# Performance work log

Hardware: AMD Instinct MI355X
Metric: run time of the kernel (lower is better)

Reference implementation:

```python
import jax, jax.numpy as jnp
import numpy as np

IN_DIM = 128
OUT_DIM = 128
NUM_RELS = 8
N_NODES = 50000
N_EDGES = 500000


def setup_inputs() -> dict:
    key = jax.random.key(0)
    k_x, k_ei_s, k_ei_d, k_et, k_w, k_sw = jax.random.split(key, 6)
    x = jax.random.normal(k_x, (N_NODES, IN_DIM), dtype=jnp.float32)
    src = jax.random.randint(k_ei_s, (N_EDGES,), 0, N_NODES)
    dst = jax.random.randint(k_ei_d, (N_EDGES,), 0, N_NODES)
    edge_index = jnp.stack([src, dst], axis=0).astype(jnp.int64)
    edge_type = jax.random.randint(k_et, (N_EDGES,), 0, NUM_RELS).astype(jnp.int64)
    # xavier_uniform: bound = sqrt(6/(fan_in+fan_out))
    bw = float(np.sqrt(6.0 / (IN_DIM + OUT_DIM)))
    weight = jax.random.uniform(k_w, (NUM_RELS, IN_DIM, OUT_DIM), dtype=jnp.float32, minval=-bw, maxval=bw)
    self_loop_weight = jax.random.uniform(k_sw, (IN_DIM, OUT_DIM), dtype=jnp.float32, minval=-bw, maxval=bw)
    bias = jnp.zeros((OUT_DIM,), dtype=jnp.float32)
    return {
        "x": x,
        "weight": weight,
        "self_loop_weight": self_loop_weight,
        "bias": bias,
        "edge_index": edge_index,
        "edge_type": edge_type,
        "num_entities": N_NODES,
    }


def reference(x, weight, self_loop_weight, bias, edge_index, edge_type, num_entities):
    # Relation-grouped formulation of the per-edge loop:
    # transform every node under every relation once: hr[r, n, o]
    hr = jnp.einsum("nd,rdo->rno", x, weight)
    src, dst = edge_index[0], edge_index[1]
    # per-edge message = x[src] @ weight[edge_type]  == hr[edge_type, src]
    msg = hr[edge_type, src]  # [E, out]
    agg = jax.ops.segment_sum(msg, dst, num_segments=num_entities)  # scatter-add into out[dst]
    out = agg + x @ self_loop_weight + bias
    return jax.nn.relu(out)
```

## Files before the change

kernel.cpp:

```cpp
#include <hip/hip_runtime.h>

#define IN_DIM 128
#define OUT_DIM 128
#define NUM_RELS 8
#define SCAN_ELEMS 2048

typedef unsigned short u16;
typedef u16 u16x8 __attribute__((ext_vector_type(8)));
typedef u16 u16x4 __attribute__((ext_vector_type(4)));
typedef __bf16 bf16x8 __attribute__((ext_vector_type(8)));
typedef float f32x4 __attribute__((ext_vector_type(4)));

__device__ __forceinline__ u16 f2bf(float f) {
    unsigned u = __float_as_uint(f);
    u += 0x7FFF + ((u >> 16) & 1);
    return (u16)(u >> 16);
}
__device__ __forceinline__ float bf2f(u16 h) {
    return __uint_as_float((unsigned)h << 16);
}

__global__ __launch_bounds__(256) void k_prep(
    const float* __restrict__ x, const float* __restrict__ weight,
    const float* __restrict__ slw,
    const int* __restrict__ dst, const int* __restrict__ et,
    u16* __restrict__ xb, u16* __restrict__ WbT, int* __restrict__ cursor,
    int N, int E, int BA, int BB)
{
    const int b = blockIdx.x;
    const int tid = threadIdx.x;
    if (b < BA) {
        long i = ((long)b * 256 + tid) * 4;
        if (i < (long)N * 128) {
            float4 v = *(const float4*)(x + i);
            u16x4 o;
            o[0] = f2bf(v.x); o[1] = f2bf(v.y); o[2] = f2bf(v.z); o[3] = f2bf(v.w);
            *(u16x4*)(xb + i) = o;
        }
    } else if (b < BA + BB) {
        int i = ((b - BA) * 256 + tid) * 4;
        if (i < 128 * 1152) {
            const int col = i / 1152;
            const int kk  = i - col * 1152;
            u16x4 o;
            #pragma unroll
            for (int j = 0; j < 4; ++j) {
                const int kj = kk + j;
                const float f = (kj < 1024)
                    ? weight[((kj >> 7) << 14) + ((kj & 127) << 7) + col]
                    : slw[((kj - 1024) << 7) + col];
                o[j] = f2bf(f);
            }
            *(u16x4*)(WbT + i) = o;
        }
    } else {
        int e = (b - BA - BB) * 256 + tid;
        if (e < E) atomicAdd(&cursor[(dst[e] << 3) + et[e]], 1);
    }
}

__global__ __launch_bounds__(256) void k_scan1(
    const int* __restrict__ deg, int* __restrict__ local,
    int* __restrict__ bsum, int n)
{
    __shared__ int s[256];
    const int t = threadIdx.x;
    const int base = blockIdx.x * SCAN_ELEMS + t * 8;
    int v[8];
    int sum = 0;
    #pragma unroll
    for (int j = 0; j < 8; ++j) {
        int i = base + j;
        v[j] = (i < n) ? deg[i] : 0;
        sum += v[j];
    }
    s[t] = sum;
    __syncthreads();
    #pragma unroll
    for (int off = 1; off < 256; off <<= 1) {
        int y = (t >= off) ? s[t - off] : 0;
        __syncthreads();
        s[t] += y;
        __syncthreads();
    }
    int run = s[t] - sum;
    #pragma unroll
    for (int j = 0; j < 8; ++j) {
        int i = base + j;
        if (i < n) local[i] = run;
        run += v[j];
    }
    if (t == 255) bsum[blockIdx.x] = s[255];
}

__global__ __launch_bounds__(256) void k_scan23(
    int* __restrict__ row_ptr, const int* __restrict__ bsum,
    int* __restrict__ cursor, int B, int n)
{
    __shared__ int s[256];
    const int t = threadIdx.x;
    int v = (t < B) ? bsum[t] : 0;
    s[t] = v;
    __syncthreads();
    #pragma unroll
    for (int off = 1; off < 256; off <<= 1) {
        int y = (t >= off) ? s[t - off] : 0;
        __syncthreads();
        s[t] += y;
        __syncthreads();
    }
    const int myoff = (blockIdx.x == 0) ? 0 : s[blockIdx.x - 1];
    const int total = s[255];
    const int base = blockIdx.x * SCAN_ELEMS + t * 8;
    #pragma unroll
    for (int j = 0; j < 8; ++j) {
        int i = base + j;
        if (i < n) {
            int val = row_ptr[i] + myoff;
            row_ptr[i] = val;
            cursor[i] = val;
        }
    }
    if (blockIdx.x == 0 && t == 0) row_ptr[n] = total;
}

__global__ __launch_bounds__(256) void k_fill(
    const int* __restrict__ src, const int* __restrict__ dst,
    const int* __restrict__ et, int* __restrict__ cursor,
    int* __restrict__ packed, int E)
{
    int e = blockIdx.x * blockDim.x + threadIdx.x;
    if (e >= E) return;
    int pos = atomicAdd(&cursor[(dst[e] << 3) + et[e]], 1);
    packed[pos] = (et[e] << 17) | src[e];
}

#define NPB 32
#define LDK 392

__global__ __launch_bounds__(512, 8) void fused_rgcn(
    const u16* __restrict__ xb,
    const u16* __restrict__ WbT,
    const float* __restrict__ bias,
    const int* __restrict__ row_ptr,
    const int* __restrict__ packed,
    float* __restrict__ out, int N)
{
    __shared__ u16 agg[NPB][LDK];

    const int tid = threadIdx.x;
    const int n0 = blockIdx.x * NPB;
    const int lane = tid & 63;
    const int wv = tid >> 6;
    const int q = lane >> 4, l = lane & 15;
    const int cbase = wv << 4;
    const int grp = tid >> 4;
    const int lo  = (tid & 15) * 8;

    const int gn = n0 + grp;
    u16* arow = &agg[grp][0];

    f32x4 acc[2] = {};

    for (int ck = 0; ck < 3; ++ck) {
        const int r0 = ck * 3;
        const int r1 = (ck == 2) ? 8 : r0 + 3;

        if (gn < N) {
            const int beg = row_ptr[(gn << 3) + r0];
            const int end = row_ptr[(gn << 3) + r1];
            float a0=0.f,a1=0.f,a2=0.f,a3=0.f,a4=0.f,a5=0.f,a6=0.f,a7=0.f;
            int cur = r0;

#define FLUSH_() { u16x8 o_; \
    o_[0]=f2bf(a0); o_[1]=f2bf(a1); o_[2]=f2bf(a2); o_[3]=f2bf(a3); \
    o_[4]=f2bf(a4); o_[5]=f2bf(a5); o_[6]=f2bf(a6); o_[7]=f2bf(a7); \
    *(u16x8*)(arow + ((cur - r0) << 7) + lo) = o_; \
    a0=0.f;a1=0.f;a2=0.f;a3=0.f;a4=0.f;a5=0.f;a6=0.f;a7=0.f; }

#define PROC_(p_, v_) { const int r_ = (p_) >> 17; \
    while (cur < r_) { FLUSH_(); ++cur; } \
    a0 += bf2f((v_)[0]); a1 += bf2f((v_)[1]); a2 += bf2f((v_)[2]); a3 += bf2f((v_)[3]); \
    a4 += bf2f((v_)[4]); a5 += bf2f((v_)[5]); a6 += bf2f((v_)[6]); a7 += bf2f((v_)[7]); }

            int k = beg;
            for (; k + 4 <= end; k += 4) {
                const int p0 = packed[k],     p1 = packed[k + 1];
                const int p2 = packed[k + 2], p3 = packed[k + 3];
                const u16x8 v0 = *(const u16x8*)(xb + ((size_t)(p0 & 0x1FFFF) << 7) + lo);
                const u16x8 v1 = *(const u16x8*)(xb + ((size_t)(p1 & 0x1FFFF) << 7) + lo);
                const u16x8 v2 = *(const u16x8*)(xb + ((size_t)(p2 & 0x1FFFF) << 7) + lo);
                const u16x8 v3 = *(const u16x8*)(xb + ((size_t)(p3 & 0x1FFFF) << 7) + lo);
                PROC_(p0, v0); PROC_(p1, v1); PROC_(p2, v2); PROC_(p3, v3);
            }
            for (; k < end; ++k) {
                const int p = packed[k];
                const u16x8 v = *(const u16x8*)(xb + ((size_t)(p & 0x1FFFF) << 7) + lo);
                PROC_(p, v);
            }
            while (cur < r1) { FLUSH_(); ++cur; }
            if (ck == 2) {
                const u16x8 sv = *(const u16x8*)(xb + ((size_t)gn << 7) + lo);
                *(u16x8*)(arow + 256 + lo) = sv;
            }
#undef PROC_
#undef FLUSH_
        }
        __syncthreads();

        const u16* Bp = WbT + (size_t)(cbase + l) * 1152 + ck * 384 + (q << 3);
        #pragma unroll
        for (int kk = 0; kk < 12; ++kk) {
            const int k0 = (kk << 5) + (q << 3);
            const bf16x8 b  = __builtin_bit_cast(bf16x8, *(const u16x8*)(Bp + (kk << 5)));
            const bf16x8 a0 = __builtin_bit_cast(bf16x8, *(const u16x8*)(&agg[l][k0]));
            const bf16x8 a1 = __builtin_bit_cast(bf16x8, *(const u16x8*)(&agg[16 + l][k0]));
            acc[0] = __builtin_amdgcn_mfma_f32_16x16x32_bf16(a0, b, acc[0], 0, 0, 0);
            acc[1] = __builtin_amdgcn_mfma_f32_16x16x32_bf16(a1, b, acc[1], 0, 0, 0);
        }
        if (ck < 2) __syncthreads();
    }

    const float bv = bias[cbase + l];
    #pragma unroll
    for (int m = 0; m < 2; ++m) {
        const int rbase = n0 + (m << 4) + (q << 2);
        #pragma unroll
        for (int j = 0; j < 4; ++j) {
            const int row = rbase + j;
            if (row < N)
                out[(size_t)row * 128 + cbase + l] = fmaxf(acc[m][j] + bv, 0.f);
        }
    }
}

__global__ __launch_bounds__(256) void gemm128(
    const float* __restrict__ x, const float* __restrict__ W,
    const float* __restrict__ bias, float* __restrict__ out, int N)
{
    __shared__ float Ws[IN_DIM * OUT_DIM];
    __shared__ float xs[16][IN_DIM];

    const float* Wz = W + (size_t)blockIdx.z * IN_DIM * OUT_DIM;
    float* outz = out + (size_t)blockIdx.z * (size_t)N * OUT_DIM;

    {
        const float4* s4 = (const float4*)Wz;
        float4* d4 = (float4*)Ws;
        for (int i = threadIdx.x; i < IN_DIM * OUT_DIM / 4; i += 256)
            d4[i] = s4[i];
    }

    const int tid = threadIdx.x;
    const int nl = (tid >> 5) * 2;
    const int og = (tid & 31) * 4;

    float4 b4 = make_float4(0.f, 0.f, 0.f, 0.f);
    if (bias) b4 = *(const float4*)&bias[og];

    const int nchunks = (N + 15) / 16;
    for (int chunk = blockIdx.x; chunk < nchunks; chunk += gridDim.x) {
        const int n0 = chunk * 16;
        const int rows = min(16, N - n0);
        __syncthreads();
        {
            const float4* xsrc = (const float4*)(x + (size_t)n0 * IN_DIM);
            float4* xdst = (float4*)&xs[0][0];
            const int n4 = rows * (IN_DIM / 4);
            for (int i = tid; i < n4; i += 256) xdst[i] = xsrc[i];
        }
        __syncthreads();

        if (nl < rows) {
            float a00 = 0.f, a01 = 0.f, a02 = 0.f, a03 = 0.f;
            float a10 = 0.f, a11 = 0.f, a12 = 0.f, a13 = 0.f;
            #pragma unroll 8
            for (int d = 0; d < IN_DIM; ++d) {
                const float4 w4 = *(const float4*)&Ws[d * OUT_DIM + og];
                const float xa = xs[nl][d];
                const float xb = xs[nl + 1][d];
                a00 += xa * w4.x; a01 += xa * w4.y; a02 += xa * w4.z; a03 += xa * w4.w;
                a10 += xb * w4.x; a11 += xb * w4.y; a12 += xb * w4.z; a13 += xb * w4.w;
            }
            float4 r0 = make_float4(a00 + b4.x, a01 + b4.y, a02 + b4.z, a03 + b4.w);
            *(float4*)&outz[(size_t)(n0 + nl) * OUT_DIM + og] = r0;
            if (nl + 1 < rows) {
                float4 r1 = make_float4(a10 + b4.x, a11 + b4.y, a12 + b4.z, a13 + b4.w);
                *(float4*)&outz[(size_t)(n0 + nl + 1) * OUT_DIM + og] = r1;
            }
        }
    }
}

__global__ __launch_bounds__(256) void edge_direct(
    const float* __restrict__ x, const float* __restrict__ W,
    const int* __restrict__ src, const int* __restrict__ dst,
    const int* __restrict__ et, float* __restrict__ out, int E)
{
    long t = (long)blockIdx.x * blockDim.x + threadIdx.x;
    long e = t >> 6;
    int lane = (int)(t & 63);
    if (e >= E) return;
    int s = src[e], d = dst[e], r = et[e];
    const float* xr = x + (long)s * IN_DIM;
    float2 xv = *(const float2*)(xr + lane * 2);
    const float* Wr = W + (long)r * IN_DIM * OUT_DIM;
    const int o0 = lane * 2;
    float a0 = 0.f, a1 = 0.f;
    #pragma unroll 8
    for (int dd = 0; dd < 64; ++dd) {
        float xa = __shfl(xv.x, dd);
        float xb = __shfl(xv.y, dd);
        a0 += xa * Wr[(2 * dd) * OUT_DIM + o0]     + xb * Wr[(2 * dd + 1) * OUT_DIM + o0];
        a1 += xa * Wr[(2 * dd) * OUT_DIM + o0 + 1] + xb * Wr[(2 * dd + 1) * OUT_DIM + o0 + 1];
    }
    atomicAdd(out + (long)d * OUT_DIM + o0, a0);
    atomicAdd(out + (long)d * OUT_DIM + o0 + 1, a1);
}

__global__ __launch_bounds__(256) void relu_k(float* __restrict__ out, long n4)
{
    long i = (long)blockIdx.x * blockDim.x + threadIdx.x;
    if (i >= n4) return;
    float4 v = ((float4*)out)[i];
    v.x = fmaxf(v.x, 0.f); v.y = fmaxf(v.y, 0.f);
    v.z = fmaxf(v.z, 0.f); v.w = fmaxf(v.w, 0.f);
    ((float4*)out)[i] = v;
}

static inline size_t align256(size_t x) { return (x + 255) & ~(size_t)255; }

extern "C" void kernel_launch(void* const* d_in, const int* in_sizes, int n_in,
                              void* d_out, int out_size, void* d_ws, size_t ws_size,
                              hipStream_t stream)
{
    const float* x      = (const float*)d_in[0];
    const float* weight = (const float*)d_in[1];
    const float* slw    = (const float*)d_in[2];
    const float* bias   = (const float*)d_in[3];
    const int*   ei     = (const int*)d_in[4];
    const int*   et     = (const int*)d_in[5];

    const int N = in_sizes[0] / IN_DIM;
    const int E = in_sizes[5];
    const int* src  = ei;
    const int* dstp = ei + E;

    float* out = (float*)d_out;

    const int n8 = N * 8;

    size_t off = 0;
    const size_t xb_off   = off; off += align256((size_t)N * 128 * 2);
    const size_t wb_off   = off; off += align256((size_t)128 * 1152 * 2);
    const size_t rp_off   = off; off += align256((size_t)(n8 + 1) * 4);
    const size_t cur_off  = off; off += align256((size_t)n8 * 4);
    const size_t pk_off   = off; off += align256((size_t)E * 4);
    const size_t bs_off   = off; off += align256(256 * 4);
    const size_t need_bf16 = off;

    const int scanB = (n8 + SCAN_ELEMS - 1) / SCAN_ELEMS;

    if (ws_size >= need_bf16 && N <= (1 << 17) && scanB <= 256) {
        char* base   = (char*)d_ws;
        u16* xb      = (u16*)(base + xb_off);
        u16* WbT     = (u16*)(base + wb_off);
        int* row_ptr = (int*)(base + rp_off);
        int* cursor  = (int*)(base + cur_off);
        int* packed  = (int*)(base + pk_off);
        int* bsum    = (int*)(base + bs_off);

        hipMemsetAsync(cursor, 0, (size_t)n8 * sizeof(int), stream);
        const int BA = (int)(((long)N * 128 / 4 + 255) / 256);
        const int BB = (128 * 1152 / 4 + 255) / 256;
        const int BD = (E + 255) / 256;
        k_prep<<<dim3(BA + BB + BD), 256, 0, stream>>>(
            x, weight, slw, dstp, et, xb, WbT, cursor, N, E, BA, BB);

        k_scan1<<<dim3(scanB), 256, 0, stream>>>(cursor, row_ptr, bsum, n8);
        k_scan23<<<dim3(scanB), 256, 0, stream>>>(row_ptr, bsum, cursor, scanB, n8);
        k_fill<<<dim3((E + 255) / 256), 256, 0, stream>>>(src, dstp, et, cursor, packed, E);

        fused_rgcn<<<dim3((N + NPB - 1) / NPB), 512, 0, stream>>>(
            xb, WbT, bias, row_ptr, packed, out, N);
    } else if (ws_size >= (size_t)NUM_RELS * N * 128 * 4) {
        gemm128<<<dim3(512, 1, 1), 256, 0, stream>>>(x, slw, bias, out, N);
        long nt = (long)E * 64;
        edge_direct<<<dim3((nt + 255) / 256), 256, 0, stream>>>(x, weight, src, dstp, et, out, E);
        long n4 = (long)N * OUT_DIM / 4;
        relu_k<<<dim3((n4 + 255) / 256), 256, 0, stream>>>(out, n4);
    } else {
        gemm128<<<dim3(512, 1, 1), 256, 0, stream>>>(x, slw, bias, out, N);
        long nt = (long)E * 64;
        edge_direct<<<dim3((nt + 255) / 256), 256, 0, stream>>>(x, weight, src, dstp, et, out, E);
        long n4 = (long)N * OUT_DIM / 4;
        relu_k<<<dim3((n4 + 255) / 256), 256, 0, stream>>>(out, n4);
    }
}
```

Measured before the change: 225.2 us.

## Fuse preprocessing, CSR build and aggregation into one cooperative persistent kernel

Replaces the memset plus five separate launches (prep, two scans, fill, fused aggregation) with a single cooperative kernel that uses grid-wide syncs between phases, saving per-launch gaps. The aggregation phase becomes persistent over node tiles and double-buffers the LDS aggregate so the gather for the next relation chunk overlaps the MFMA on the current one. The trade-offs are grid.sync costs, a grid capped at 2048 blocks with lower occupancy (launch bounds 512,6), a larger LDS footprint, and the scan being spread across fewer chunks. The old multi-kernel path is kept as a fallback if the cooperative launch fails.

```diff
diff --git a/kernel.cpp b/kernel.cpp
--- a/kernel.cpp
+++ b/kernel.cpp
@@ -1,4 +1,7 @@
 #include <hip/hip_runtime.h>
+#include <hip/hip_cooperative_groups.h>
+
+namespace cg = cooperative_groups;
 
 #define IN_DIM 128
 #define OUT_DIM 128
@@ -18,6 +21,227 @@
 }
 __device__ __forceinline__ float bf2f(u16 h) {
     return __uint_as_float((unsigned)h << 16);
+}
+
+#define NPB 32
+#define LDK 392
+
+__device__ __forceinline__ void gather_into(
+    u16* arow, const u16* __restrict__ xb, const int* __restrict__ packed,
+    int beg, int end, int r0, int r1, int lo)
+{
+    float a0=0.f,a1=0.f,a2=0.f,a3=0.f,a4=0.f,a5=0.f,a6=0.f,a7=0.f;
+    int cur = r0;
+
+#define FLUSH_() { u16x8 o_; \
+    o_[0]=f2bf(a0); o_[1]=f2bf(a1); o_[2]=f2bf(a2); o_[3]=f2bf(a3); \
+    o_[4]=f2bf(a4); o_[5]=f2bf(a5); o_[6]=f2bf(a6); o_[7]=f2bf(a7); \
+    *(u16x8*)(arow + ((cur - r0) << 7) + lo) = o_; \
+    a0=0.f;a1=0.f;a2=0.f;a3=0.f;a4=0.f;a5=0.f;a6=0.f;a7=0.f; }
+
+#define PROC_(p_, v_) { const int r_ = (p_) >> 17; \
+    while (cur < r_) { FLUSH_(); ++cur; } \
+    a0 += bf2f((v_)[0]); a1 += bf2f((v_)[1]); a2 += bf2f((v_)[2]); a3 += bf2f((v_)[3]); \
+    a4 += bf2f((v_)[4]); a5 += bf2f((v_)[5]); a6 += bf2f((v_)[6]); a7 += bf2f((v_)[7]); }
+
+    int k = beg;
+    for (; k + 4 <= end; k += 4) {
+        const int p0 = packed[k],     p1 = packed[k + 1];
+        const int p2 = packed[k + 2], p3 = packed[k + 3];
+        const u16x8 v0 = *(const u16x8*)(xb + ((size_t)(p0 & 0x1FFFF) << 7) + lo);
+        const u16x8 v1 = *(const u16x8*)(xb + ((size_t)(p1 & 0x1FFFF) << 7) + lo);
+        const u16x8 v2 = *(const u16x8*)(xb + ((size_t)(p2 & 0x1FFFF) << 7) + lo);
+        const u16x8 v3 = *(const u16x8*)(xb + ((size_t)(p3 & 0x1FFFF) << 7) + lo);
+        PROC_(p0, v0); PROC_(p1, v1); PROC_(p2, v2); PROC_(p3, v3);
+    }
+    for (; k < end; ++k) {
+        const int p = packed[k];
+        const u16x8 v = *(const u16x8*)(xb + ((size_t)(p & 0x1FFFF) << 7) + lo);
+        PROC_(p, v);
+    }
+    while (cur < r1) { FLUSH_(); ++cur; }
+#undef PROC_
+#undef FLUSH_
+}
+
+__global__ __launch_bounds__(512, 6) void mega_rgcn(
+    const float* __restrict__ x, const float* __restrict__ weight,
+    const float* __restrict__ slw, const float* __restrict__ bias,
+    const int* __restrict__ src, const int* __restrict__ dst,
+    const int* __restrict__ et,
+    u16* __restrict__ xb, u16* __restrict__ WbT,
+    int* __restrict__ row_ptr, int* __restrict__ cursor,
+    int* __restrict__ packed, int* __restrict__ bsum,
+    float* __restrict__ out,
+    int N, int E, int n8, int ntiles)
+{
+    __shared__ u16 agg[2][NPB][LDK];
+    __shared__ int s[512];
+
+    cg::grid_group grid = cg::this_grid();
+
+    const int tid = threadIdx.x;
+    const int gtid = blockIdx.x * 512 + tid;
+    const int gstride = gridDim.x * 512;
+
+    {
+        const int xq = N * 32;
+        const int wq = 128 * 1152 / 4;
+        const int cq = n8 >> 2;
+        const int tot = xq + wq + cq;
+        for (int i = gtid; i < tot; i += gstride) {
+            if (i < xq) {
+                const int e = i << 2;
+                const float4 v = *(const float4*)(x + e);
+                u16x4 o;
+                o[0]=f2bf(v.x); o[1]=f2bf(v.y); o[2]=f2bf(v.z); o[3]=f2bf(v.w);
+                *(u16x4*)(xb + e) = o;
+            } else if (i < xq + wq) {
+                const int ii = (i - xq) << 2;
+                const int col = ii / 1152;
+                const int kk  = ii - col * 1152;
+                u16x4 o;
+                #pragma unroll
+                for (int j = 0; j < 4; ++j) {
+                    const int kj = kk + j;
+                    const float f = (kj < 1024)
+                        ? weight[((kj >> 7) << 14) + ((kj & 127) << 7) + col]
+                        : slw[((kj - 1024) << 7) + col];
+                    o[j] = f2bf(f);
+                }
+                *(u16x4*)(WbT + ii) = o;
+            } else {
+                const int ii = (i - xq - wq) << 2;
+                *(int4*)(cursor + ii) = make_int4(0, 0, 0, 0);
+            }
+        }
+        if (gtid == 0) row_ptr[n8] = E;
+    }
+    grid.sync();
+
+    for (int e = gtid; e < E; e += gstride)
+        atomicAdd(&cursor[(dst[e] << 3) + et[e]], 1);
+    grid.sync();
+
+    const int nchunks = (n8 + 4095) >> 12;
+    for (int c = blockIdx.x; c < nchunks; c += gridDim.x) {
+        const int base = (c << 12) + (tid << 3);
+        int v[8]; int sum = 0;
+        #pragma unroll
+        for (int j = 0; j < 8; ++j) {
+            const int i = base + j;
+            v[j] = (i < n8) ? cursor[i] : 0;
+            sum += v[j];
+        }
+        s[tid] = sum;
+        __syncthreads();
+        #pragma unroll
+        for (int off = 1; off < 512; off <<= 1) {
+            const int y = (tid >= off) ? s[tid - off] : 0;
+            __syncthreads();
+            s[tid] += y;
+            __syncthreads();
+        }
+        int run = s[tid] - sum;
+        #pragma unroll
+        for (int j = 0; j < 8; ++j) {
+            const int i = base + j;
+            if (i < n8) row_ptr[i] = run;
+            run += v[j];
+        }
+        if (tid == 511) bsum[c] = s[511];
+        __syncthreads();
+    }
+    grid.sync();
+
+    for (int c = blockIdx.x; c < nchunks; c += gridDim.x) {
+        if (tid < 256) s[tid] = (tid < nchunks) ? bsum[tid] : 0;
+        __syncthreads();
+        #pragma unroll
+        for (int off = 1; off < 256; off <<= 1) {
+            int y = 0;
+            if (tid < 256 && tid >= off) y = s[tid - off];
+            __syncthreads();
+            if (tid < 256) s[tid] += y;
+            __syncthreads();
+        }
+        const int myoff = (c == 0) ? 0 : s[c - 1];
+        const int base = (c << 12) + (tid << 3);
+        #pragma unroll
+        for (int j = 0; j < 8; ++j) {
+            const int i = base + j;
+            if (i < n8) {
+                const int val = row_ptr[i] + myoff;
+                row_ptr[i] = val;
+                cursor[i] = val;
+            }
+        }
+        __syncthreads();
+    }
+    grid.sync();
+
+    for (int e = gtid; e < E; e += gstride) {
+        const int pos = atomicAdd(&cursor[(dst[e] << 3) + et[e]], 1);
+        packed[pos] = (et[e] << 17) | src[e];
+    }
+    grid.sync();
+
+    const int lane = tid & 63;
+    const int wv = tid >> 6;
+    const int q = lane >> 4, l = lane & 15;
+    const int cbase = wv << 4;
+    const int grp = tid >> 4;
+    const int lo  = (tid & 15) * 8;
+    const float bv = bias[cbase + l];
+
+    for (int tile = blockIdx.x; tile < ntiles; tile += gridDim.x) {
+        const int n0 = tile * NPB;
+        const int gn = n0 + grp;
+        int rp0 = 0, rp3 = 0, rp6 = 0, rp8 = 0;
+        if (gn < N) {
+            const int rb = gn << 3;
+            rp0 = row_ptr[rb];     rp3 = row_ptr[rb + 3];
+            rp6 = row_ptr[rb + 6]; rp8 = row_ptr[rb + 8];
+        }
+        f32x4 acc[2] = {};
+
+        if (gn < N) gather_into(&agg[0][grp][0], xb, packed, rp0, rp3, 0, 3, lo);
+        __syncthreads();
+
+        #pragma unroll
+        for (int ck = 0; ck < 3; ++ck) {
+            if (ck == 0 && gn < N)
+                gather_into(&agg[1][grp][0], xb, packed, rp3, rp6, 3, 6, lo);
+            if (ck == 1 && gn < N) {
+                gather_into(&agg[0][grp][0], xb, packed, rp6, rp8, 6, 8, lo);
+                const u16x8 sv = *(const u16x8*)(xb + ((size_t)gn << 7) + lo);
+                *(u16x8*)(&agg[0][grp][0] + 256 + lo) = sv;
+            }
+            const u16* Bp = WbT + (size_t)(cbase + l) * 1152 + ck * 384 + (q << 3);
+            u16 (*ab)[LDK] = agg[ck & 1];
+            #pragma unroll
+            for (int kk = 0; kk < 12; ++kk) {
+                const int k0 = (kk << 5) + (q << 3);
+                const bf16x8 b  = __builtin_bit_cast(bf16x8, *(const u16x8*)(Bp + (kk << 5)));
+                const bf16x8 a0 = __builtin_bit_cast(bf16x8, *(const u16x8*)(&ab[l][k0]));
+                const bf16x8 a1 = __builtin_bit_cast(bf16x8, *(const u16x8*)(&ab[16 + l][k0]));
+                acc[0] = __builtin_amdgcn_mfma_f32_16x16x32_bf16(a0, b, acc[0], 0, 0, 0);
+                acc[1] = __builtin_amdgcn_mfma_f32_16x16x32_bf16(a1, b, acc[1], 0, 0, 0);
+            }
+            __syncthreads();
+        }
+
+        #pragma unroll
+        for (int m = 0; m < 2; ++m) {
+            const int rbase = n0 + (m << 4) + (q << 2);
+            #pragma unroll
+            for (int j = 0; j < 4; ++j) {
+                const int row = rbase + j;
+                if (row < N)
+                    out[(size_t)row * 128 + cbase + l] = fmaxf(acc[m][j] + bv, 0.f);
+            }
+        }
+    }
 }
 
 __global__ __launch_bounds__(256) void k_prep(
@@ -135,15 +359,10 @@
     packed[pos] = (et[e] << 17) | src[e];
 }
 
-#define NPB 32
-#define LDK 392
-
 __global__ __launch_bounds__(512, 8) void fused_rgcn(
-    const u16* __restrict__ xb,
-    const u16* __restrict__ WbT,
+    const u16* __restrict__ xb, const u16* __restrict__ WbT,
     const float* __restrict__ bias,
-    const int* __restrict__ row_ptr,
-    const int* __restrict__ packed,
+    const int* __restrict__ row_ptr, const int* __restrict__ packed,
     float* __restrict__ out, int N)
 {
     __shared__ u16 agg[NPB][LDK];
@@ -165,46 +384,14 @@
     for (int ck = 0; ck < 3; ++ck) {
         const int r0 = ck * 3;
         const int r1 = (ck == 2) ? 8 : r0 + 3;
-
         if (gn < N) {
             const int beg = row_ptr[(gn << 3) + r0];
             const int end = row_ptr[(gn << 3) + r1];
-            float a0=0.f,a1=0.f,a2=0.f,a3=0.f,a4=0.f,a5=0.f,a6=0.f,a7=0.f;
-            int cur = r0;
-
-#define FLUSH_() { u16x8 o_; \
-    o_[0]=f2bf(a0); o_[1]=f2bf(a1); o_[2]=f2bf(a2); o_[3]=f2bf(a3); \
-    o_[4]=f2bf(a4); o_[5]=f2bf(a5); o_[6]=f2bf(a6); o_[7]=f2bf(a7); \
-    *(u16x8*)(arow + ((cur - r0) << 7) + lo) = o_; \
-    a0=0.f;a1=0.f;a2=0.f;a3=0.f;a4=0.f;a5=0.f;a6=0.f;a7=0.f; }
-
-#define PROC_(p_, v_) { const int r_ = (p_) >> 17; \
-    while (cur < r_) { FLUSH_(); ++cur; } \
-    a0 += bf2f((v_)[0]); a1 += bf2f((v_)[1]); a2 += bf2f((v_)[2]); a3 += bf2f((v_)[3]); \
-    a4 += bf2f((v_)[4]); a5 += bf2f((v_)[5]); a6 += bf2f((v_)[6]); a7 += bf2f((v_)[7]); }
-
-            int k = beg;
-            for (; k + 4 <= end; k += 4) {
-                const int p0 = packed[k],     p1 = packed[k + 1];
-                const int p2 = packed[k + 2], p3 = packed[k + 3];
-                const u16x8 v0 = *(const u16x8*)(xb + ((size_t)(p0 & 0x1FFFF) << 7) + lo);
-                const u16x8 v1 = *(const u16x8*)(xb + ((size_t)(p1 & 0x1FFFF) << 7) + lo);
-                const u16x8 v2 = *(const u16x8*)(xb + ((size_t)(p2 & 0x1FFFF) << 7) + lo);
-                const u16x8 v3 = *(const u16x8*)(xb + ((size_t)(p3 & 0x1FFFF) << 7) + lo);
-                PROC_(p0, v0); PROC_(p1, v1); PROC_(p2, v2); PROC_(p3, v3);
-            }
-            for (; k < end; ++k) {
-                const int p = packed[k];
-                const u16x8 v = *(const u16x8*)(xb + ((size_t)(p & 0x1FFFF) << 7) + lo);
-                PROC_(p, v);
-            }
-            while (cur < r1) { FLUSH_(); ++cur; }
+            gather_into(arow, xb, packed, beg, end, r0, r1, lo);
             if (ck == 2) {
                 const u16x8 sv = *(const u16x8*)(xb + ((size_t)gn << 7) + lo);
                 *(u16x8*)(arow + 256 + lo) = sv;
             }
-#undef PROC_
-#undef FLUSH_
         }
         __syncthreads();
 
@@ -370,19 +557,54 @@
         int* packed  = (int*)(base + pk_off);
         int* bsum    = (int*)(base + bs_off);
 
-        hipMemsetAsync(cursor, 0, (size_t)n8 * sizeof(int), stream);
-        const int BA = (int)(((long)N * 128 / 4 + 255) / 256);
-        const int BB = (128 * 1152 / 4 + 255) / 256;
-        const int BD = (E + 255) / 256;
-        k_prep<<<dim3(BA + BB + BD), 256, 0, stream>>>(
-            x, weight, slw, dstp, et, xb, WbT, cursor, N, E, BA, BB);
-
-        k_scan1<<<dim3(scanB), 256, 0, stream>>>(cursor, row_ptr, bsum, n8);
-        k_scan23<<<dim3(scanB), 256, 0, stream>>>(row_ptr, bsum, cursor, scanB, n8);
-        k_fill<<<dim3((E + 255) / 256), 256, 0, stream>>>(src, dstp, et, cursor, packed, E);
-
-        fused_rgcn<<<dim3((N + NPB - 1) / NPB), 512, 0, stream>>>(
-            xb, WbT, bias, row_ptr, packed, out, N);
+        const int ntiles = (N + NPB - 1) / NPB;
+
+        static int s_G = -2;
+        if (s_G == -2) {
+            int dev = 0;
+            (void)hipGetDevice(&dev);
+            int ncu = 0;
+            if (hipDeviceGetAttribute(&ncu, hipDeviceAttributeMultiprocessorCount,
+                                      dev) != hipSuccess || ncu <= 0)
+                ncu = 256;
+            int maxb = 0;
+            if (hipOccupancyMaxActiveBlocksPerMultiprocessor(
+                    &maxb, reinterpret_cast<const void*>(&mega_rgcn), 512, 0)
+                    != hipSuccess)
+                maxb = 0;
+            s_G = (maxb >= 1) ? ((ncu * maxb > 2048) ? 2048 : ncu * maxb) : -1;
+        }
+
+        bool launched = false;
+        if (s_G > 0) {
+            int Nv = N, Ev = E, n8v = n8, ntv = ntiles;
+            void* args[] = {
+                (void*)&x, (void*)&weight, (void*)&slw, (void*)&bias,
+                (void*)&src, (void*)&dstp, (void*)&et,
+                (void*)&xb, (void*)&WbT, (void*)&row_ptr, (void*)&cursor,
+                (void*)&packed, (void*)&bsum, (void*)&out,
+                (void*)&Nv, (void*)&Ev, (void*)&n8v, (void*)&ntv
+            };
+            hipError_t err = hipLaunchCooperativeKernel(
+                reinterpret_cast<const void*>(&mega_rgcn),
+                dim3(s_G), dim3(512), args, 0, stream);
+            if (err == hipSuccess) launched = true;
+            else s_G = -1;
+        }
+
+        if (!launched) {
+            hipMemsetAsync(cursor, 0, (size_t)n8 * sizeof(int), stream);
+            const int BA = (int)(((long)N * 128 / 4 + 255) / 256);
+            const int BB = (128 * 1152 / 4 + 255) / 256;
+            const int BD = (E + 255) / 256;
+            k_prep<<<dim3(BA + BB + BD), 256, 0, stream>>>(
+                x, weight, slw, dstp, et, xb, WbT, cursor, N, E, BA, BB);
+            k_scan1<<<dim3(scanB), 256, 0, stream>>>(cursor, row_ptr, bsum, n8);
+            k_scan23<<<dim3(scanB), 256, 0, stream>>>(row_ptr, bsum, cursor, scanB, n8);
+            k_fill<<<dim3((E + 255) / 256), 256, 0, stream>>>(src, dstp, et, cursor, packed, E);
+            fused_rgcn<<<dim3((N + NPB - 1) / NPB), 512, 0, stream>>>(
+                xb, WbT, bias, row_ptr, packed, out, N);
+        }
     } else if (ws_size >= (size_t)NUM_RELS * N * 128 * 4) {
         gemm128<<<dim3(512, 1, 1), 256, 0, stream>>>(x, slw, bias, out, N);
         long nt = (long)E * 64;
```

Result: slower. 437.8 us (+94.4%).

## Double-buffer gather/MFMA in persistent RGCN kernel and use single-pass lookback scan

Applied to the files above, without the earlier changes.

The two-kernel block scan is replaced by one single-pass scan that chains chunk prefixes through decoupled lookback via atomic flags in a partials buffer. The row_ptr tail is now written in the prep kernel. The fused RGCN kernel becomes persistent, with a grid capped at 768 blocks and double-buffered LDS, so the gather for the next relation chunk or next tile overlaps the MFMA on the current one. In exchange, LDS use per block doubles and launch bounds drop to 6 blocks per CU, and with only about two tiles per block the overlap benefit may be limited.

```diff
diff --git a/kernel.cpp b/kernel.cpp
--- a/kernel.cpp
+++ b/kernel.cpp
@@ -3,7 +3,6 @@
 #define IN_DIM 128
 #define OUT_DIM 128
 #define NUM_RELS 8
-#define SCAN_ELEMS 2048
 
 typedef unsigned short u16;
 typedef u16 u16x8 __attribute__((ext_vector_type(8)));
@@ -25,10 +24,12 @@
     const float* __restrict__ slw,
     const int* __restrict__ dst, const int* __restrict__ et,
     u16* __restrict__ xb, u16* __restrict__ WbT, int* __restrict__ cursor,
-    int N, int E, int BA, int BB)
+    int* __restrict__ row_ptr,
+    int N, int E, int n8, int BA, int BB)
 {
     const int b = blockIdx.x;
     const int tid = threadIdx.x;
+    if (b == 0 && tid == 0) row_ptr[n8] = E;
     if (b < BA) {
         long i = ((long)b * 256 + tid) * 4;
         if (i < (long)N * 128) {
@@ -59,69 +60,81 @@
     }
 }
 
-__global__ __launch_bounds__(256) void k_scan1(
-    const int* __restrict__ deg, int* __restrict__ local,
-    int* __restrict__ bsum, int n)
-{
-    __shared__ int s[256];
+__global__ __launch_bounds__(512) void k_scan_lb(
+    const int* __restrict__ deg, int* __restrict__ row_ptr,
+    int* __restrict__ cursor, unsigned long long* __restrict__ part, int n)
+{
+    __shared__ int s[512];
+    __shared__ int s_exc;
+    const int c = blockIdx.x;
     const int t = threadIdx.x;
-    const int base = blockIdx.x * SCAN_ELEMS + t * 8;
-    int v[8];
-    int sum = 0;
+    const int base = (c << 12) + (t << 3);
+    int v[8]; int sum = 0;
     #pragma unroll
     for (int j = 0; j < 8; ++j) {
-        int i = base + j;
+        const int i = base + j;
         v[j] = (i < n) ? deg[i] : 0;
         sum += v[j];
     }
     s[t] = sum;
     __syncthreads();
     #pragma unroll
-    for (int off = 1; off < 256; off <<= 1) {
-        int y = (t >= off) ? s[t - off] : 0;
+    for (int off = 1; off < 512; off <<= 1) {
+        const int y = (t >= off) ? s[t - off] : 0;
         __syncthreads();
         s[t] += y;
         __syncthreads();
     }
-    int run = s[t] - sum;
+    const int total = s[511];
+    const int run = s[t] - sum;
+
+    if (t == 0) {
+        const unsigned long long st = (c == 0) ? 2ULL : 1ULL;
+        __hip_atomic_store(&part[c], (st << 32) | (unsigned int)total,
+                           __ATOMIC_RELAXED, __HIP_MEMORY_SCOPE_AGENT);
+    }
+
+    int exc = 0;
+    if (c > 0 && t < 64) {
+        int bj = c - 1;
+        while (true) {
+            const int idx = bj - t;
+            unsigned long long w = 0;
+            if (idx >= 0) {
+                do {
+                    w = __hip_atomic_load(&part[idx], __ATOMIC_RELAXED,
+                                          __HIP_MEMORY_SCOPE_AGENT);
+                } while ((w >> 32) == 0ULL);
+            }
+            const unsigned long long incmask =
+                __ballot(idx >= 0 && (w >> 32) == 2ULL);
+            const int Ls = incmask ? (__ffsll(incmask) - 1) : 64;
+            unsigned int contrib =
+                (idx >= 0 && t <= Ls) ? (unsigned int)(w & 0xffffffffULL) : 0u;
+            #pragma unroll
+            for (int o = 32; o >= 1; o >>= 1) contrib += __shfl_xor(contrib, o);
+            exc += (int)contrib;
+            if (Ls < 64) break;
+            bj -= 64;
+        }
+        if (t == 0) {
+            __hip_atomic_store(&part[c],
+                (2ULL << 32) | (unsigned int)(exc + total),
+                __ATOMIC_RELAXED, __HIP_MEMORY_SCOPE_AGENT);
+            s_exc = exc;
+        }
+    } else if (t == 0) {
+        s_exc = 0;
+    }
+    __syncthreads();
+    exc = s_exc;
+    int acc_ = exc + run;
     #pragma unroll
     for (int j = 0; j < 8; ++j) {
-        int i = base + j;
-        if (i < n) local[i] = run;
-        run += v[j];
-    }
-    if (t == 255) bsum[blockIdx.x] = s[255];
-}
-
-__global__ __launch_bounds__(256) void k_scan23(
-    int* __restrict__ row_ptr, const int* __restrict__ bsum,
-    int* __restrict__ cursor, int B, int n)
-{
-    __shared__ int s[256];
-    const int t = threadIdx.x;
-    int v = (t < B) ? bsum[t] : 0;
-    s[t] = v;
-    __syncthreads();
-    #pragma unroll
-    for (int off = 1; off < 256; off <<= 1) {
-        int y = (t >= off) ? s[t - off] : 0;
-        __syncthreads();
-        s[t] += y;
-        __syncthreads();
-    }
-    const int myoff = (blockIdx.x == 0) ? 0 : s[blockIdx.x - 1];
-    const int total = s[255];
-    const int base = blockIdx.x * SCAN_ELEMS + t * 8;
-    #pragma unroll
-    for (int j = 0; j < 8; ++j) {
-        int i = base + j;
-        if (i < n) {
-            int val = row_ptr[i] + myoff;
-            row_ptr[i] = val;
-            cursor[i] = val;
-        }
-    }
-    if (blockIdx.x == 0 && t == 0) row_ptr[n] = total;
+        const int i = base + j;
+        if (i < n) { row_ptr[i] = acc_; cursor[i] = acc_; }
+        acc_ += v[j];
+    }
 }
 
 __global__ __launch_bounds__(256) void k_fill(
@@ -138,99 +151,130 @@
 #define NPB 32
 #define LDK 392
 
-__global__ __launch_bounds__(512, 8) void fused_rgcn(
+__device__ __forceinline__ void gather_into(
+    u16* arow, const u16* __restrict__ xb, const int* __restrict__ packed,
+    int beg, int end, int r0, int r1, int lo)
+{
+    float a0=0.f,a1=0.f,a2=0.f,a3=0.f,a4=0.f,a5=0.f,a6=0.f,a7=0.f;
+    int cur = r0;
+
+#define FLUSH_() { u16x8 o_; \
+    o_[0]=f2bf(a0); o_[1]=f2bf(a1); o_[2]=f2bf(a2); o_[3]=f2bf(a3); \
+    o_[4]=f2bf(a4); o_[5]=f2bf(a5); o_[6]=f2bf(a6); o_[7]=f2bf(a7); \
+    *(u16x8*)(arow + ((cur - r0) << 7) + lo) = o_; \
+    a0=0.f;a1=0.f;a2=0.f;a3=0.f;a4=0.f;a5=0.f;a6=0.f;a7=0.f; }
+
+#define PROC_(p_, v_) { const int r_ = (p_) >> 17; \
+    while (cur < r_) { FLUSH_(); ++cur; } \
+    a0 += bf2f((v_)[0]); a1 += bf2f((v_)[1]); a2 += bf2f((v_)[2]); a3 += bf2f((v_)[3]); \
+    a4 += bf2f((v_)[4]); a5 += bf2f((v_)[5]); a6 += bf2f((v_)[6]); a7 += bf2f((v_)[7]); }
+
+    int k = beg;
+    for (; k + 4 <= end; k += 4) {
+        const int p0 = packed[k],     p1 = packed[k + 1];
+        const int p2 = packed[k + 2], p3 = packed[k + 3];
+        const u16x8 v0 = *(const u16x8*)(xb + ((size_t)(p0 & 0x1FFFF) << 7) + lo);
+        const u16x8 v1 = *(const u16x8*)(xb + ((size_t)(p1 & 0x1FFFF) << 7) + lo);
+        const u16x8 v2 = *(const u16x8*)(xb + ((size_t)(p2 & 0x1FFFF) << 7) + lo);
+        const u16x8 v3 = *(const u16x8*)(xb + ((size_t)(p3 & 0x1FFFF) << 7) + lo);
+        PROC_(p0, v0); PROC_(p1, v1); PROC_(p2, v2); PROC_(p3, v3);
+    }
+    for (; k < end; ++k) {
+        const int p = packed[k];
+        const u16x8 v = *(const u16x8*)(xb + ((size_t)(p & 0x1FFFF) << 7) + lo);
+        PROC_(p, v);
+    }
+    while (cur < r1) { FLUSH_(); ++cur; }
+#undef PROC_
+#undef FLUSH_
+}
+
+__global__ __launch_bounds__(512, 6) void fused_rgcn(
     const u16* __restrict__ xb,
     const u16* __restrict__ WbT,
     const float* __restrict__ bias,
     const int* __restrict__ row_ptr,
     const int* __restrict__ packed,
-    float* __restrict__ out, int N)
-{
-    __shared__ u16 agg[NPB][LDK];
+    float* __restrict__ out, int N, int ntiles)
+{
+    __shared__ u16 agg[2][NPB][LDK];
 
     const int tid = threadIdx.x;
-    const int n0 = blockIdx.x * NPB;
     const int lane = tid & 63;
     const int wv = tid >> 6;
     const int q = lane >> 4, l = lane & 15;
     const int cbase = wv << 4;
     const int grp = tid >> 4;
     const int lo  = (tid & 15) * 8;
-
-    const int gn = n0 + grp;
-    u16* arow = &agg[grp][0];
-
-    f32x4 acc[2] = {};
-
-    for (int ck = 0; ck < 3; ++ck) {
-        const int r0 = ck * 3;
-        const int r1 = (ck == 2) ? 8 : r0 + 3;
-
-        if (gn < N) {
-            const int beg = row_ptr[(gn << 3) + r0];
-            const int end = row_ptr[(gn << 3) + r1];
-            float a0=0.f,a1=0.f,a2=0.f,a3=0.f,a4=0.f,a5=0.f,a6=0.f,a7=0.f;
-            int cur = r0;
-
-#define FLUSH_() { u16x8 o_; \
-    o_[0]=f2bf(a0); o_[1]=f2bf(a1); o_[2]=f2bf(a2); o_[3]=f2bf(a3); \
-    o_[4]=f2bf(a4); o_[5]=f2bf(a5); o_[6]=f2bf(a6); o_[7]=f2bf(a7); \
-    *(u16x8*)(arow + ((cur - r0) << 7) + lo) = o_; \
-    a0=0.f;a1=0.f;a2=0.f;a3=0.f;a4=0.f;a5=0.f;a6=0.f;a7=0.f; }
-
-#define PROC_(p_, v_) { const int r_ = (p_) >> 17; \
-    while (cur < r_) { FLUSH_(); ++cur; } \
-    a0 += bf2f((v_)[0]); a1 += bf2f((v_)[1]); a2 += bf2f((v_)[2]); a3 += bf2f((v_)[3]); \
-    a4 += bf2f((v_)[4]); a5 += bf2f((v_)[5]); a6 += bf2f((v_)[6]); a7 += bf2f((v_)[7]); }
-
-            int k = beg;
-            for (; k + 4 <= end; k += 4) {
-                const int p0 = packed[k],     p1 = packed[k + 1];
-                const int p2 = packed[k + 2], p3 = packed[k + 3];
-                const u16x8 v0 = *(const u16x8*)(xb + ((size_t)(p0 & 0x1FFFF) << 7) + lo);
-                const u16x8 v1 = *(const u16x8*)(xb + ((size_t)(p1 & 0x1FFFF) << 7) + lo);
-                const u16x8 v2 = *(const u16x8*)(xb + ((size_t)(p2 & 0x1FFFF) << 7) + lo);
-                const u16x8 v3 = *(const u16x8*)(xb + ((size_t)(p3 & 0x1FFFF) << 7) + lo);
-                PROC_(p0, v0); PROC_(p1, v1); PROC_(p2, v2); PROC_(p3, v3);
-            }
-            for (; k < end; ++k) {
-                const int p = packed[k];
-                const u16x8 v = *(const u16x8*)(xb + ((size_t)(p & 0x1FFFF) << 7) + lo);
-                PROC_(p, v);
-            }
-            while (cur < r1) { FLUSH_(); ++cur; }
-            if (ck == 2) {
-                const u16x8 sv = *(const u16x8*)(xb + ((size_t)gn << 7) + lo);
-                *(u16x8*)(arow + 256 + lo) = sv;
-            }
-#undef PROC_
-#undef FLUSH_
-        }
-        __syncthreads();
-
-        const u16* Bp = WbT + (size_t)(cbase + l) * 1152 + ck * 384 + (q << 3);
+    const float bv = bias[cbase + l];
+    const int gstride = gridDim.x;
+
+    int tile = blockIdx.x;
+    int gn = tile * NPB + grp;
+    int rp0 = 0, rp3 = 0, rp6 = 0, rp8 = 0;
+    if (gn < N) {
+        const int rb = gn << 3;
+        rp0 = row_ptr[rb];     rp3 = row_ptr[rb + 3];
+        rp6 = row_ptr[rb + 6]; rp8 = row_ptr[rb + 8];
+    }
+    if (gn < N) gather_into(&agg[0][grp][0], xb, packed, rp0, rp3, 0, 3, lo);
+    __syncthreads();
+    int pb = 1;
+
+    for (; tile < ntiles; tile += gstride) {
+        const int tn = tile + gstride;
+        int nrp0 = 0, nrp3 = 0, nrp6 = 0, nrp8 = 0, ngn = N;
+        if (tn < ntiles) {
+            ngn = tn * NPB + grp;
+            if (ngn < N) {
+                const int rb = ngn << 3;
+                nrp0 = row_ptr[rb];     nrp3 = row_ptr[rb + 3];
+                nrp6 = row_ptr[rb + 6]; nrp8 = row_ptr[rb + 8];
+            }
+        }
+        f32x4 acc[2] = {};
+
         #pragma unroll
-        for (int kk = 0; kk < 12; ++kk) {
-            const int k0 = (kk << 5) + (q << 3);
-            const bf16x8 b  = __builtin_bit_cast(bf16x8, *(const u16x8*)(Bp + (kk << 5)));
-            const bf16x8 a0 = __builtin_bit_cast(bf16x8, *(const u16x8*)(&agg[l][k0]));
-            const bf16x8 a1 = __builtin_bit_cast(bf16x8, *(const u16x8*)(&agg[16 + l][k0]));
-            acc[0] = __builtin_amdgcn_mfma_f32_16x16x32_bf16(a0, b, acc[0], 0, 0, 0);
-            acc[1] = __builtin_amdgcn_mfma_f32_16x16x32_bf16(a1, b, acc[1], 0, 0, 0);
-        }
-        if (ck < 2) __syncthreads();
-    }
-
-    const float bv = bias[cbase + l];
-    #pragma unroll
-    for (int m = 0; m < 2; ++m) {
-        const int rbase = n0 + (m << 4) + (q << 2);
+        for (int ck = 0; ck < 3; ++ck) {
+            if (ck == 0) {
+                if (gn < N)
+                    gather_into(&agg[pb][grp][0], xb, packed, rp3, rp6, 3, 6, lo);
+            } else if (ck == 1) {
+                if (gn < N) {
+                    gather_into(&agg[pb][grp][0], xb, packed, rp6, rp8, 6, 8, lo);
+                    const u16x8 sv = *(const u16x8*)(xb + ((size_t)gn << 7) + lo);
+                    *(u16x8*)(&agg[pb][grp][0] + 256 + lo) = sv;
+                }
+            } else {
+                if (tn < ntiles && ngn < N)
+                    gather_into(&agg[pb][grp][0], xb, packed, nrp0, nrp3, 0, 3, lo);
+            }
+            const u16* Bp = WbT + (size_t)(cbase + l) * 1152 + ck * 384 + (q << 3);
+            u16 (*ab)[LDK] = agg[pb ^ 1];
+            #pragma unroll
+            for (int kk = 0; kk < 12; ++kk) {
+                const int k0 = (kk << 5) + (q << 3);
+                const bf16x8 b  = __builtin_bit_cast(bf16x8, *(const u16x8*)(Bp + (kk << 5)));
+                const bf16x8 a0 = __builtin_bit_cast(bf16x8, *(const u16x8*)(&ab[l][k0]));
+                const bf16x8 a1 = __builtin_bit_cast(bf16x8, *(const u16x8*)(&ab[16 + l][k0]));
+                acc[0] = __builtin_amdgcn_mfma_f32_16x16x32_bf16(a0, b, acc[0], 0, 0, 0);
+                acc[1] = __builtin_amdgcn_mfma_f32_16x16x32_bf16(a1, b, acc[1], 0, 0, 0);
+            }
+            __syncthreads();
+            pb ^= 1;
+        }
+
         #pragma unroll
-        for (int j = 0; j < 4; ++j) {
-            const int row = rbase + j;
-            if (row < N)
-                out[(size_t)row * 128 + cbase + l] = fmaxf(acc[m][j] + bv, 0.f);
-        }
+        for (int m = 0; m < 2; ++m) {
+            const int rbase = tile * NPB + (m << 4) + (q << 2);
+            #pragma unroll
+            for (int j = 0; j < 4; ++j) {
+                const int row = rbase + j;
+                if (row < N)
+                    out[(size_t)row * 128 + cbase + l] = fmaxf(acc[m][j] + bv, 0.f);
+            }
+        }
+        gn = ngn; rp0 = nrp0; rp3 = nrp3; rp6 = nrp6; rp8 = nrp8;
     }
 }
 
@@ -355,34 +399,36 @@
     const size_t wb_off   = off; off += align256((size_t)128 * 1152 * 2);
     const size_t rp_off   = off; off += align256((size_t)(n8 + 1) * 4);
     const size_t cur_off  = off; off += align256((size_t)n8 * 4);
+    const size_t pt_off   = off; off += align256(256 * 8);
     const size_t pk_off   = off; off += align256((size_t)E * 4);
-    const size_t bs_off   = off; off += align256(256 * 4);
     const size_t need_bf16 = off;
 
-    const int scanB = (n8 + SCAN_ELEMS - 1) / SCAN_ELEMS;
-
-    if (ws_size >= need_bf16 && N <= (1 << 17) && scanB <= 256) {
+    const int nchunks = (n8 + 4095) >> 12;
+
+    if (ws_size >= need_bf16 && N <= (1 << 17) && nchunks <= 256) {
         char* base   = (char*)d_ws;
         u16* xb      = (u16*)(base + xb_off);
         u16* WbT     = (u16*)(base + wb_off);
         int* row_ptr = (int*)(base + rp_off);
         int* cursor  = (int*)(base + cur_off);
+        unsigned long long* part = (unsigned long long*)(base + pt_off);
         int* packed  = (int*)(base + pk_off);
-        int* bsum    = (int*)(base + bs_off);
-
-        hipMemsetAsync(cursor, 0, (size_t)n8 * sizeof(int), stream);
+
+        hipMemsetAsync(base + cur_off, 0, (pt_off - cur_off) + 256 * 8, stream);
+
         const int BA = (int)(((long)N * 128 / 4 + 255) / 256);
         const int BB = (128 * 1152 / 4 + 255) / 256;
         const int BD = (E + 255) / 256;
         k_prep<<<dim3(BA + BB + BD), 256, 0, stream>>>(
-            x, weight, slw, dstp, et, xb, WbT, cursor, N, E, BA, BB);
-
-        k_scan1<<<dim3(scanB), 256, 0, stream>>>(cursor, row_ptr, bsum, n8);
-        k_scan23<<<dim3(scanB), 256, 0, stream>>>(row_ptr, bsum, cursor, scanB, n8);
+            x, weight, slw, dstp, et, xb, WbT, cursor, row_ptr, N, E, n8, BA, BB);
+
+        k_scan_lb<<<dim3(nchunks), 512, 0, stream>>>(cursor, row_ptr, cursor, part, n8);
         k_fill<<<dim3((E + 255) / 256), 256, 0, stream>>>(src, dstp, et, cursor, packed, E);
 
-        fused_rgcn<<<dim3((N + NPB - 1) / NPB), 512, 0, stream>>>(
-            xb, WbT, bias, row_ptr, packed, out, N);
+        const int ntiles = (N + NPB - 1) / NPB;
+        const int G = ntiles < 768 ? ntiles : 768;
+        fused_rgcn<<<dim3(G), 512, 0, stream>>>(
+            xb, WbT, bias, row_ptr, packed, out, N, ntiles);
     } else if (ws_size >= (size_t)NUM_RELS * N * 128 * 4) {
         gemm128<<<dim3(512, 1, 1), 256, 0, stream>>>(x, slw, bias, out, N);
         long nt = (long)E * 64;
```

Result: slower. 320.0 us (+42.1%).
